# Performance work log

Hardware: AMD Instinct MI355X
Metric: run time of the kernel (lower is better)

## Reference

```python
import jax, jax.numpy as jnp
import numpy as np

B, N, DIM = 8, 8192, 512
H, DH = 8, 64
INNER = H * DH
EPS = 1e-5


def setup_inputs() -> dict:
    key = jax.random.key(0)
    ks = jax.random.split(key, 5)
    x = jax.random.normal(ks[0], (B, N, DIM), dtype=jnp.float32)
    w_qkv = jax.random.normal(ks[1], (DIM, 3 * INNER), dtype=jnp.float32) * (DIM ** -0.5)
    ln_w = jnp.ones((INNER,), dtype=jnp.float32)
    ln_b = jnp.zeros((INNER,), dtype=jnp.float32)
    w_out = jax.random.normal(ks[2], (INNER, DIM), dtype=jnp.float32) * (INNER ** -0.5)
    b_out = jnp.zeros((DIM,), dtype=jnp.float32)
    return {"x": x, "w_qkv": w_qkv, "ln_w": ln_w, "ln_b": ln_b,
            "w_out": w_out, "b_out": b_out}


def _layernorm(x, w, b):
    mu = jnp.mean(x, axis=-1, keepdims=True)
    var = jnp.mean(jnp.square(x - mu), axis=-1, keepdims=True)
    return (x - mu) * jax.lax.rsqrt(var + EPS) * w + b


def reference(x, w_qkv, ln_w, ln_b, w_out, b_out):
    b, n, _ = x.shape
    qkv = x @ w_qkv  # [b, n, 3*inner]
    q, k, v = jnp.split(qkv, 3, axis=-1)
    # b n (h d) -> b h n d
    def heads(t):
        return t.reshape(b, n, H, DH).transpose(0, 2, 1, 3)
    q, k, v = heads(q), heads(k), heads(v)
    q = jax.nn.relu(q)
    k = jax.nn.relu(k)
    kv = jnp.einsum('bhnm,bhnd->bhmd', k, v)   # [b, h, d, d]
    out = jnp.einsum('bhnm,bhmd->bhnd', q, kv)  # [b, h, n, d]
    out = out.transpose(0, 2, 1, 3).reshape(b, n, INNER)
    out = _layernorm(out, ln_w, ln_b)
    return out @ w_out + b_out
```

## Files before the change

kernel.cpp:

```cpp
#include <hip/hip_runtime.h>
#include <stdint.h>

#define B_ 8
#define N_ 8192
#define DIM_ 512
#define H_ 8
#define DH_ 64
#define ROWS (B_*N_)
#define TRIPLE (3*DIM_)
#define EPS_ 1e-5f

typedef __attribute__((ext_vector_type(8))) short short8;
typedef __attribute__((ext_vector_type(4))) float f32x4;
typedef __attribute__((ext_vector_type(4))) float fl4;
typedef __attribute__((ext_vector_type(4))) unsigned short us4;
typedef __attribute__((ext_vector_type(8))) unsigned short us8;

#define AS1 __attribute__((address_space(1)))
#define AS3 __attribute__((address_space(3)))

__device__ __forceinline__ void gld16(const void* g, void* l) {
    __builtin_amdgcn_global_load_lds((const AS1 void*)(uintptr_t)g,
                                     (AS3 void*)(unsigned)(uintptr_t)l, 16, 0, 0);
}

__device__ inline unsigned short f2bf(float f) {
    union { float f; unsigned int u; } x; x.f = f;
    unsigned int r = x.u + 0x7fffu + ((x.u >> 16) & 1u);
    return (unsigned short)(r >> 16);
}
__device__ inline float bf2f(unsigned short b) {
    union { unsigned int u; float f; } x; x.u = ((unsigned int)b) << 16;
    return x.f;
}

__device__ __forceinline__ int eoff(int row, int col) {
    return row * 64 + (col ^ ((((unsigned)row >> 2) & 3) << 4));
}

__global__ __launch_bounds__(256) void k_cvt(const float* __restrict__ x,
                                             unsigned short* __restrict__ xb) {
    size_t i = ((size_t)blockIdx.x * 256 + threadIdx.x) * 8;
    fl4 a = *(const fl4*)(x + i);
    fl4 b = *(const fl4*)(x + i + 4);
    us8 r;
    r[0] = f2bf(a[0]); r[1] = f2bf(a[1]); r[2] = f2bf(a[2]); r[3] = f2bf(a[3]);
    r[4] = f2bf(b[0]); r[5] = f2bf(b[1]); r[6] = f2bf(b[2]); r[7] = f2bf(b[3]);
    *(us8*)(xb + i) = r;
}

__global__ __launch_bounds__(256) void k_prep(const float* __restrict__ wq,
        const float* __restrict__ wo,
        unsigned short* __restrict__ wqT, unsigned short* __restrict__ woT) {
    __shared__ float T[32][33];
    int bid = blockIdx.x;
    const float* src; unsigned short* dst; int srcCols, dstCols, k0, n0;
    if (bid < 768) {
        int tn = bid % 48, tk = bid / 48;
        src = wq; dst = wqT; srcCols = 1536; dstCols = 512;
        k0 = tk * 32; n0 = tn * 32;
    } else {
        int b = bid - 768;
        int tn = b % 16, tk = b / 16;
        src = wo; dst = woT; srcCols = 512; dstCols = 512;
        k0 = tk * 32; n0 = tn * 32;
    }
    int t = threadIdx.x, r = t >> 3, c4 = (t & 7) * 4;
    fl4 v = *(const fl4*)(src + (size_t)(k0 + r) * srcCols + n0 + c4);
    T[c4 + 0][r] = v[0]; T[c4 + 1][r] = v[1];
    T[c4 + 2][r] = v[2]; T[c4 + 3][r] = v[3];
    __syncthreads();
    us4 o;
    o[0] = f2bf(T[r][c4 + 0]); o[1] = f2bf(T[r][c4 + 1]);
    o[2] = f2bf(T[r][c4 + 2]); o[3] = f2bf(T[r][c4 + 3]);
    *(us4*)(dst + (size_t)(n0 + r) * dstCols + k0 + c4) = o;
}

__global__ __launch_bounds__(512, 4) void k_qkv8(const unsigned short* __restrict__ xb,
        const unsigned short* __restrict__ wT,
        unsigned short* __restrict__ qkv)
{
    __shared__ __align__(1024) unsigned short LDSb[3][12288];

    const int tid  = threadIdx.x;
    const int lane = tid & 63;
    const int wid  = tid >> 6;
    const int wr   = wid >> 1;
    const int wc   = wid & 1;
    const int lr   = lane & 15;

    int id  = blockIdx.x;
    int nid = (id & 7) * 384 + (id >> 3);
    int n0  = (nid % 12) * 128;
    int m0  = (nid / 12) * 256;

    const unsigned short* pA[2];
    const unsigned short* pB1;
    unsigned ldstA[2], ldstB;
#pragma unroll
    for (int j = 0; j < 2; ++j) {
        int s    = tid + j * 512;
        int row  = ((s >> 6) << 4) + ((s >> 2) & 15);
        int colb = ((s & 3) << 4) ^ (((s >> 5) & 1) << 5);
        pA[j] = xb + (size_t)(m0 + row) * 512 + (colb >> 1);
        ldstA[j] = (unsigned)((j * 512 + wid * 64) * 8);
    }
    {
        int s    = tid;
        int row  = ((s >> 6) << 4) + ((s >> 2) & 15);
        int colb = ((s & 3) << 4) ^ (((s >> 5) & 1) << 5);
        pB1 = wT + (size_t)(n0 + row) * 512 + (colb >> 1);
        ldstB = (unsigned)(8192 + wid * 64 * 8);
    }
    const int kg = (lane >> 4) * 8;
    const int lo = lr * 32 + (kg ^ ((lr >> 3) << 4));

    auto STAGE = [&](int t, int slot) {
        gld16(pA[0] + t * 32, (void*)&LDSb[slot][ldstA[0]]);
        gld16(pA[1] + t * 32, (void*)&LDSb[slot][ldstA[1]]);
        gld16(pB1   + t * 32, (void*)&LDSb[slot][ldstB]);
    };

    f32x4 acc[4][4] = {};
    short8 af[4], bfr[4];

    STAGE(0, 0);
    STAGE(1, 1);

#define WAITV(n) asm volatile("s_waitcnt vmcnt(" #n ")" ::: "memory")
#pragma unroll
    for (int t = 0; t < 16; ++t) {
        if (t <= 14) WAITV(3);
        else         WAITV(0);
        __builtin_amdgcn_s_barrier();
        __builtin_amdgcn_sched_barrier(0);

        if (t + 2 < 16) STAGE(t + 2, (t + 2) % 3);

        const unsigned short* L = LDSb[t % 3];
#pragma unroll
        for (int m = 0; m < 4; ++m)
            af[m] = *(const short8*)&L[(wr * 4 + m) * 512 + lo];
#pragma unroll
        for (int n = 0; n < 4; ++n)
            bfr[n] = *(const short8*)&L[8192 + (wc * 4 + n) * 512 + lo];

        __builtin_amdgcn_s_setprio(1);
#pragma unroll
        for (int m = 0; m < 4; ++m)
#pragma unroll
            for (int n = 0; n < 4; ++n)
                acc[m][n] = __builtin_amdgcn_mfma_f32_16x16x32_bf16(af[m], bfr[n], acc[m][n], 0, 0, 0);
        __builtin_amdgcn_s_setprio(0);
    }
#undef WAITV

    __syncthreads();

    unsigned short* S = ((unsigned short*)LDSb) + wid * 4096;
    const bool relu_tile = (n0 < 1024);
#pragma unroll
    for (int m = 0; m < 4; ++m) {
        int rbase = m * 16 + ((lane >> 4) << 2);
#pragma unroll
        for (int n = 0; n < 4; ++n) {
            int col = n * 16 + lr;
#pragma unroll
            for (int r = 0; r < 4; ++r) {
                float v = acc[m][n][r];
                if (relu_tile && v < 0.0f) v = 0.0f;
                S[eoff(rbase + r, col)] = f2bf(v);
            }
        }
    }
    __syncthreads();
    {
        int rsub = lane >> 3, sub = lane & 7;
        size_t grow = (size_t)(m0 + wr * 64);
        int gcol = n0 + wc * 64 + sub * 8;
#pragma unroll
        for (int rd = 0; rd < 8; ++rd) {
            int row = rd * 8 + rsub;
            short8 vv = *(const short8*)&S[eoff(row, sub * 8)];
            *(short8*)(qkv + (grow + row) * TRIPLE + gcol) = vv;
        }
    }
}

__global__ __launch_bounds__(256) void k_qkv_f(const float* __restrict__ x,
        const unsigned short* __restrict__ wT,
        unsigned short* __restrict__ qkv)
{
    __shared__ unsigned short As[128][40];
    __shared__ unsigned short Bs[128][40];
    int t = threadIdx.x;
    int lane = t & 63, wave = t >> 6;
    int m0 = blockIdx.y * 128;
    int n0 = blockIdx.x * 128;
    int wm = (wave & 1) * 64, wn = (wave >> 1) * 64;
    int lr = lane & 15, kg = (lane >> 4) * 8;

    f32x4 acc[4][4] = {};
    for (int k0 = 0; k0 < DIM_; k0 += 32) {
#pragma unroll
        for (int i = 0; i < 4; ++i) {
            int c = t + 256 * i;
            int r = c >> 3, c4 = (c & 7) * 4;
            fl4 v = *(const fl4*)(x + (size_t)(m0 + r) * DIM_ + k0 + c4);
            unsigned short* dst = &As[r][c4];
            dst[0] = f2bf(v[0]); dst[1] = f2bf(v[1]); dst[2] = f2bf(v[2]); dst[3] = f2bf(v[3]);
        }
#pragma unroll
        for (int i = 0; i < 2; ++i) {
            int c = t + 256 * i;
            int r = c >> 2, c8 = (c & 3) * 8;
            *(int4*)&Bs[r][c8] = *(const int4*)(wT + (size_t)(n0 + r) * DIM_ + k0 + c8);
        }
        __syncthreads();
        short8 af[4], bfr[4];
#pragma unroll
        for (int i = 0; i < 4; ++i) af[i]  = *(short8*)&As[wm + i*16 + lr][kg];
#pragma unroll
        for (int j = 0; j < 4; ++j) bfr[j] = *(short8*)&Bs[wn + j*16 + lr][kg];
#pragma unroll
        for (int i = 0; i < 4; ++i)
#pragma unroll
            for (int j = 0; j < 4; ++j)
                acc[i][j] = __builtin_amdgcn_mfma_f32_16x16x32_bf16(af[i], bfr[j], acc[i][j], 0, 0, 0);
        __syncthreads();
    }
#pragma unroll
    for (int i = 0; i < 4; ++i) {
        int row = m0 + wm + i*16 + (lane >> 4) * 4;
#pragma unroll
        for (int j = 0; j < 4; ++j) {
            int col = n0 + wn + j*16 + (lane & 15);
            bool rl = (col < 1024);
#pragma unroll
            for (int r = 0; r < 4; ++r) {
                float v = acc[i][j][r];
                if (rl && v < 0.0f) v = 0.0f;
                qkv[(size_t)(row + r) * TRIPLE + col] = f2bf(v);
            }
        }
    }
}

__global__ __launch_bounds__(256) void k_kv(const unsigned short* __restrict__ qkv,
                                            float* __restrict__ kv)
{
    __shared__ unsigned short KT[64][136];
    __shared__ unsigned short VT[64][136];
    __shared__ float red[64 * 64];
    int t = threadIdx.x, lane = t & 63, wave = t >> 6;
    int bh = blockIdx.x;
    int b = bh >> 3, h = bh & 7;
    int chunk = blockIdx.y;
    size_t rowbase = (size_t)b * N_ + (size_t)chunk * 1024;
    int kcol = DIM_ + h * 64;
    int vcol = 2 * DIM_ + h * 64;
    int lr = lane & 15;

    f32x4 acc[4][4] = {};
    for (int tile = 0; tile < 8; ++tile) {
        size_t r0 = rowbase + tile * 128;
#pragma unroll
        for (int i = 0; i < 2; ++i) {
            int u = t + 256 * i;
            int rp = u >> 3;
            int c8 = (u & 7) * 8;
            size_t ra = r0 + 2 * rp, rb = ra + 1;
            us8 ka = *(const us8*)(qkv + ra * TRIPLE + kcol + c8);
            us8 kb = *(const us8*)(qkv + rb * TRIPLE + kcol + c8);
            us8 va = *(const us8*)(qkv + ra * TRIPLE + vcol + c8);
            us8 vb = *(const us8*)(qkv + rb * TRIPLE + vcol + c8);
#pragma unroll
            for (int j = 0; j < 8; ++j) {
                int d = c8 + j;
                *(unsigned int*)&KT[d][2 * rp] =
                    (unsigned int)ka[j] | ((unsigned int)kb[j] << 16);
                *(unsigned int*)&VT[d][2 * rp] =
                    (unsigned int)va[j] | ((unsigned int)vb[j] << 16);
            }
        }
        __syncthreads();
        int kg = wave * 32 + (lane >> 4) * 8;
        short8 af[4], bfr[4];
#pragma unroll
        for (int i = 0; i < 4; ++i) af[i]  = *(short8*)&KT[i*16 + lr][kg];
#pragma unroll
        for (int j = 0; j < 4; ++j) bfr[j] = *(short8*)&VT[j*16 + lr][kg];
#pragma unroll
        for (int i = 0; i < 4; ++i)
#pragma unroll
            for (int j = 0; j < 4; ++j)
                acc[i][j] = __builtin_amdgcn_mfma_f32_16x16x32_bf16(af[i], bfr[j], acc[i][j], 0, 0, 0);
        __syncthreads();
    }
    for (int w = 0; w < 4; ++w) {
        if (wave == w) {
#pragma unroll
            for (int i = 0; i < 4; ++i)
#pragma unroll
                for (int j = 0; j < 4; ++j)
#pragma unroll
                    for (int r = 0; r < 4; ++r) {
                        int m = i*16 + (lane >> 4) * 4 + r;
                        int d = j*16 + (lane & 15);
                        if (w == 0) red[m * 64 + d] = acc[i][j][r];
                        else        red[m * 64 + d] += acc[i][j][r];
                    }
        }
        __syncthreads();
    }
    float* kvout = kv + (size_t)bh * 4096;
#pragma unroll
    for (int i = 0; i < 16; ++i) {
        int idx = t + 256 * i;
        atomicAdd(&kvout[idx], red[idx]);
    }
}

__global__ __launch_bounds__(256) void k_kvt(const float* __restrict__ kv,
                                             unsigned short* __restrict__ kvtb) {
    __shared__ float T[64][65];
    int bh = blockIdx.x, t = threadIdx.x;
    const float* src = kv + (size_t)bh * 4096;
    unsigned short* dst = kvtb + (size_t)bh * 4096;
#pragma unroll
    for (int i = 0; i < 16; ++i) {
        int idx = t + 256 * i;
        T[idx & 63][idx >> 6] = src[idx];
    }
    __syncthreads();
#pragma unroll
    for (int i = 0; i < 16; ++i) {
        int idx = t + 256 * i;
        dst[idx] = f2bf(T[idx >> 6][idx & 63]);
    }
}

__global__ __launch_bounds__(256) void k_attn(unsigned short* __restrict__ qkv,
                                              const unsigned short* __restrict__ kvtb,
                                              const float* __restrict__ lnw,
                                              const float* __restrict__ lnb)
{
    __shared__ unsigned short Qh[128][72];
    __shared__ unsigned short kvT[64][72];
    __shared__ __align__(64) unsigned short Sout[128 * 64];
    __shared__ float muS[128], rsS[128];
    int t = threadIdx.x, lane = t & 63, wave = t >> 6;
    size_t r0 = (size_t)blockIdx.x * 128;
    int b = (int)(r0 / N_);
    int lr = lane & 15;

    float lw8[8], lb8[8];
#pragma unroll
    for (int j = 0; j < 8; ++j) { lw8[j] = lnw[lane * 8 + j]; lb8[j] = lnb[lane * 8 + j]; }

    float s8[8] = {}, ss8[8] = {};

    for (int h = 0; h < H_; ++h) {
#pragma unroll
        for (int i = 0; i < 4; ++i) {
            int c = t + 256 * i;
            int r = c >> 3, f8 = (c & 7) * 8;
            *(us8*)&Qh[r][f8] = *(const us8*)(qkv + (r0 + r) * TRIPLE + h * 64 + f8);
        }
        const unsigned short* kvh = kvtb + (size_t)(b * 8 + h) * 4096;
#pragma unroll
        for (int i = 0; i < 2; ++i) {
            int c = t + 256 * i;
            int d = c >> 3, m8 = (c & 7) * 8;
            *(us8*)&kvT[d][m8] = *(const us8*)(kvh + d * 64 + m8);
        }
        __syncthreads();
        f32x4 acc[2][4] = {};
#pragma unroll
        for (int ks = 0; ks < 2; ++ks) {
            int kg = ks * 32 + (lane >> 4) * 8;
            short8 af[2], bfr[4];
#pragma unroll
            for (int i = 0; i < 2; ++i) af[i]  = *(short8*)&Qh[wave*32 + i*16 + lr][kg];
#pragma unroll
            for (int j = 0; j < 4; ++j) bfr[j] = *(short8*)&kvT[j*16 + lr][kg];
#pragma unroll
            for (int i = 0; i < 2; ++i)
#pragma unroll
                for (int j = 0; j < 4; ++j)
                    acc[i][j] = __builtin_amdgcn_mfma_f32_16x16x32_bf16(af[i], bfr[j], acc[i][j], 0, 0, 0);
        }
#pragma unroll
        for (int i = 0; i < 2; ++i)
#pragma unroll
            for (int j = 0; j < 4; ++j) {
                int rbase = wave*32 + i*16 + (lane >> 4) * 4;
                int col = j*16 + lr;
#pragma unroll
                for (int r = 0; r < 4; ++r) {
                    float v = acc[i][j][r];
                    s8[i*4+r]  += v;
                    ss8[i*4+r] += v * v;
                    Sout[eoff(rbase + r, col)] = f2bf(v);
                }
            }
        __syncthreads();
        {
            int sub = t & 7, rsub = t >> 3;
#pragma unroll
            for (int rd = 0; rd < 4; ++rd) {
                int row = rd * 32 + rsub;
                short8 vv = *(const short8*)&Sout[eoff(row, sub * 8)];
                *(short8*)(qkv + (r0 + row) * TRIPLE + h * 64 + sub * 8) = vv;
            }
        }
        __syncthreads();
    }

#pragma unroll
    for (int q = 0; q < 8; ++q) {
        float s = s8[q], ss = ss8[q];
        s += __shfl_xor(s, 1);  ss += __shfl_xor(ss, 1);
        s += __shfl_xor(s, 2);  ss += __shfl_xor(ss, 2);
        s += __shfl_xor(s, 4);  ss += __shfl_xor(ss, 4);
        s += __shfl_xor(s, 8);  ss += __shfl_xor(ss, 8);
        s8[q] = s; ss8[q] = ss;
    }
    if (lr == 0) {
#pragma unroll
        for (int q = 0; q < 8; ++q) {
            int row = wave*32 + (q >> 2)*16 + (lane >> 4)*4 + (q & 3);
            float m = s8[q] * (1.0f / 512.0f);
            muS[row] = m;
            rsS[row] = rsqrtf(ss8[q] * (1.0f / 512.0f) - m * m + EPS_);
        }
    }
    __syncthreads();

#pragma unroll
    for (int i = 0; i < 32; ++i) {
        int row = wave + 4 * i;
        unsigned short* p = qkv + (r0 + row) * TRIPLE + lane * 8;
        us8 v = *(const us8*)p;
        float mm = muS[row], rr = rsS[row];
        us8 o;
#pragma unroll
        for (int j = 0; j < 8; ++j)
            o[j] = f2bf((bf2f(v[j]) - mm) * rr * lw8[j] + lb8[j]);
        *(us8*)p = o;
    }
}

__global__ __launch_bounds__(256) void k_out(const unsigned short* __restrict__ qkv,
        const unsigned short* __restrict__ woutT,
        const float* __restrict__ bout, float* __restrict__ out)
{
    __shared__ unsigned short As[128][40];
    __shared__ unsigned short Bs[128][40];
    int t = threadIdx.x, lane = t & 63, wave = t >> 6;
    int id  = blockIdx.y * 4 + blockIdx.x;
    int nid = (id & 7) * 256 + (id >> 3);
    int m0  = (nid >> 2) * 128;
    int n0  = (nid & 3) * 128;
    int wm = (wave & 1) * 64, wn = (wave >> 1) * 64;
    int lr = lane & 15, kg = (lane >> 4) * 8;

    f32x4 acc[4][4] = {};
    for (int k0 = 0; k0 < 512; k0 += 32) {
#pragma unroll
        for (int i = 0; i < 2; ++i) {
            int c = t + 256 * i;
            int r = c >> 2, c8 = (c & 3) * 8;
            *(int4*)&As[r][c8] = *(const int4*)(qkv + (size_t)(m0 + r) * TRIPLE + k0 + c8);
        }
#pragma unroll
        for (int i = 0; i < 2; ++i) {
            int c = t + 256 * i;
            int r = c >> 2, c8 = (c & 3) * 8;
            *(int4*)&Bs[r][c8] = *(const int4*)(woutT + (size_t)(n0 + r) * DIM_ + k0 + c8);
        }
        __syncthreads();
        short8 af[4], bfr[4];
#pragma unroll
        for (int i = 0; i < 4; ++i) af[i]  = *(short8*)&As[wm + i*16 + lr][kg];
#pragma unroll
        for (int j = 0; j < 4; ++j) bfr[j] = *(short8*)&Bs[wn + j*16 + lr][kg];
#pragma unroll
        for (int i = 0; i < 4; ++i)
#pragma unroll
            for (int j = 0; j < 4; ++j)
                acc[i][j] = __builtin_amdgcn_mfma_f32_16x16x32_bf16(af[i], bfr[j], acc[i][j], 0, 0, 0);
        __syncthreads();
    }
#pragma unroll
    for (int i = 0; i < 4; ++i) {
        int row = m0 + wm + i*16 + (lane >> 4) * 4;
#pragma unroll
        for (int j = 0; j < 4; ++j) {
            int col = n0 + wn + j*16 + (lane & 15);
            float bo = bout[col];
#pragma unroll
            for (int r = 0; r < 4; ++r)
                out[(size_t)(row + r) * DIM_ + col] = acc[i][j][r] + bo;
        }
    }
}

extern "C" void kernel_launch(void* const* d_in, const int* in_sizes, int n_in,
                              void* d_out, int out_size, void* d_ws, size_t ws_size,
                              hipStream_t stream) {
    (void)in_sizes; (void)n_in; (void)out_size;
    const float* x     = (const float*)d_in[0];
    const float* w_qkv = (const float*)d_in[1];
    const float* ln_w  = (const float*)d_in[2];
    const float* ln_b  = (const float*)d_in[3];
    const float* w_out = (const float*)d_in[4];
    const float* b_out = (const float*)d_in[5];
    float* out = (float*)d_out;

    char* ws = (char*)d_ws;
    const size_t QKV_BYTES = (size_t)ROWS * TRIPLE * sizeof(unsigned short);
    const size_t KV_BYTES  = (size_t)64 * 64 * 64 * sizeof(float);
    const size_t WQT_BYTES = (size_t)TRIPLE * DIM_ * sizeof(unsigned short);
    const size_t WOT_BYTES = (size_t)DIM_ * DIM_ * sizeof(unsigned short);
    const size_t KVT_BYTES = (size_t)64 * 64 * 64 * sizeof(unsigned short);
    const size_t XB_BYTES  = (size_t)ROWS * DIM_ * sizeof(unsigned short);
    unsigned short* qkv   = (unsigned short*)ws;
    float*          kvbuf = (float*)(ws + QKV_BYTES);
    unsigned short* wqkvT = (unsigned short*)(ws + QKV_BYTES + KV_BYTES);
    unsigned short* woutT = (unsigned short*)(ws + QKV_BYTES + KV_BYTES + WQT_BYTES);
    unsigned short* kvtb  = (unsigned short*)(ws + QKV_BYTES + KV_BYTES + WQT_BYTES + WOT_BYTES);
    unsigned short* xb    = (unsigned short*)(ws + QKV_BYTES + KV_BYTES + WQT_BYTES + WOT_BYTES + KVT_BYTES);
    const size_t NEED = QKV_BYTES + KV_BYTES + WQT_BYTES + WOT_BYTES + KVT_BYTES + XB_BYTES;

    hipMemsetAsync(kvbuf, 0, KV_BYTES, stream);
    k_prep<<<1024, 256, 0, stream>>>(w_qkv, w_out, wqkvT, woutT);
    if (ws_size >= NEED) {
        k_cvt<<<16384, 256, 0, stream>>>(x, xb);
        k_qkv8<<<dim3(3072), 512, 0, stream>>>(xb, wqkvT, qkv);
    } else {
        k_qkv_f<<<dim3(12, 512), 256, 0, stream>>>(x, wqkvT, qkv);
    }
    k_kv<<<dim3(64, 8), 256, 0, stream>>>(qkv, kvbuf);
    k_kvt<<<64, 256, 0, stream>>>(kvbuf, kvtb);
    k_attn<<<512, 256, 0, stream>>>(qkv, kvtb, ln_w, ln_b);
    k_out<<<dim3(4, 512), 256, 0, stream>>>(qkv, woutT, b_out, out);
}
```

Baseline: 525.8 us.

## Fuse attention output, layernorm and output projection into one kernel

Merges k_attn and k_out into a single kernel. Each 128-row block keeps its full 128x512 attention output in a swizzled LDS buffer, applies layernorm in place, then runs the output GEMM against w_out read straight from global memory. This removes the write and re-read of the normalized activations through qkv and one kernel launch. In exchange it uses 128KB+ of LDS per block, so occupancy drops to about one block per CU. Q, kv and w_out fragments are now loaded from global memory directly rather than staged through shared memory.

```diff
diff --git a/kernel.cpp b/kernel.cpp
--- a/kernel.cpp
+++ b/kernel.cpp
@@ -36,6 +36,10 @@
 
 __device__ __forceinline__ int eoff(int row, int col) {
     return row * 64 + (col ^ ((((unsigned)row >> 2) & 3) << 4));
+}
+
+__device__ __forceinline__ int aoff(int row, int col) {
+    return row * 512 + ((((col >> 3) ^ (row & 7)) << 3) | (col & 7));
 }
 
 __global__ __launch_bounds__(256) void k_cvt(const float* __restrict__ x,
@@ -340,50 +344,38 @@
     }
 }
 
-__global__ __launch_bounds__(256) void k_attn(unsigned short* __restrict__ qkv,
-                                              const unsigned short* __restrict__ kvtb,
-                                              const float* __restrict__ lnw,
-                                              const float* __restrict__ lnb)
+__global__ __launch_bounds__(256) void k_ao(
+        const unsigned short* __restrict__ qkv,
+        const unsigned short* __restrict__ kvtb,
+        const float* __restrict__ lnw, const float* __restrict__ lnb,
+        const unsigned short* __restrict__ woutT,
+        const float* __restrict__ bout, float* __restrict__ out)
 {
-    __shared__ unsigned short Qh[128][72];
-    __shared__ unsigned short kvT[64][72];
-    __shared__ __align__(64) unsigned short Sout[128 * 64];
-    __shared__ float muS[128], rsS[128];
+    __shared__ unsigned short attnS[128 * 512];
+    __shared__ float lwS[512], lbS[512], muS[128], rsS[128];
     int t = threadIdx.x, lane = t & 63, wave = t >> 6;
+    int lr = lane & 15;
     size_t r0 = (size_t)blockIdx.x * 128;
     int b = (int)(r0 / N_);
-    int lr = lane & 15;
-
-    float lw8[8], lb8[8];
-#pragma unroll
-    for (int j = 0; j < 8; ++j) { lw8[j] = lnw[lane * 8 + j]; lb8[j] = lnb[lane * 8 + j]; }
+
+    for (int i = t; i < 512; i += 256) { lwS[i] = lnw[i]; lbS[i] = lnb[i]; }
 
     float s8[8] = {}, ss8[8] = {};
 
+#pragma unroll
     for (int h = 0; h < H_; ++h) {
-#pragma unroll
-        for (int i = 0; i < 4; ++i) {
-            int c = t + 256 * i;
-            int r = c >> 3, f8 = (c & 7) * 8;
-            *(us8*)&Qh[r][f8] = *(const us8*)(qkv + (r0 + r) * TRIPLE + h * 64 + f8);
-        }
         const unsigned short* kvh = kvtb + (size_t)(b * 8 + h) * 4096;
-#pragma unroll
-        for (int i = 0; i < 2; ++i) {
-            int c = t + 256 * i;
-            int d = c >> 3, m8 = (c & 7) * 8;
-            *(us8*)&kvT[d][m8] = *(const us8*)(kvh + d * 64 + m8);
-        }
-        __syncthreads();
         f32x4 acc[2][4] = {};
 #pragma unroll
         for (int ks = 0; ks < 2; ++ks) {
             int kg = ks * 32 + (lane >> 4) * 8;
             short8 af[2], bfr[4];
 #pragma unroll
-            for (int i = 0; i < 2; ++i) af[i]  = *(short8*)&Qh[wave*32 + i*16 + lr][kg];
-#pragma unroll
-            for (int j = 0; j < 4; ++j) bfr[j] = *(short8*)&kvT[j*16 + lr][kg];
+            for (int i = 0; i < 2; ++i)
+                af[i] = *(const short8*)(qkv + (r0 + wave * 32 + i * 16 + lr) * TRIPLE + h * 64 + kg);
+#pragma unroll
+            for (int j = 0; j < 4; ++j)
+                bfr[j] = *(const short8*)(kvh + (j * 16 + lr) * 64 + kg);
 #pragma unroll
             for (int i = 0; i < 2; ++i)
 #pragma unroll
@@ -394,27 +386,16 @@
         for (int i = 0; i < 2; ++i)
 #pragma unroll
             for (int j = 0; j < 4; ++j) {
-                int rbase = wave*32 + i*16 + (lane >> 4) * 4;
-                int col = j*16 + lr;
+                int rbase = wave * 32 + i * 16 + (lane >> 4) * 4;
+                int col = h * 64 + j * 16 + lr;
 #pragma unroll
                 for (int r = 0; r < 4; ++r) {
                     float v = acc[i][j][r];
-                    s8[i*4+r]  += v;
-                    ss8[i*4+r] += v * v;
-                    Sout[eoff(rbase + r, col)] = f2bf(v);
+                    s8[i * 4 + r] += v;
+                    ss8[i * 4 + r] += v * v;
+                    attnS[aoff(rbase + r, col)] = f2bf(v);
                 }
             }
-        __syncthreads();
-        {
-            int sub = t & 7, rsub = t >> 3;
-#pragma unroll
-            for (int rd = 0; rd < 4; ++rd) {
-                int row = rd * 32 + rsub;
-                short8 vv = *(const short8*)&Sout[eoff(row, sub * 8)];
-                *(short8*)(qkv + (r0 + row) * TRIPLE + h * 64 + sub * 8) = vv;
-            }
-        }
-        __syncthreads();
     }
 
 #pragma unroll
@@ -429,7 +410,7 @@
     if (lr == 0) {
 #pragma unroll
         for (int q = 0; q < 8; ++q) {
-            int row = wave*32 + (q >> 2)*16 + (lane >> 4)*4 + (q & 3);
+            int row = wave * 32 + (q >> 2) * 16 + (lane >> 4) * 4 + (q & 3);
             float m = s8[q] * (1.0f / 512.0f);
             muS[row] = m;
             rsS[row] = rsqrtf(ss8[q] * (1.0f / 512.0f) - m * m + EPS_);
@@ -437,71 +418,55 @@
     }
     __syncthreads();
 
-#pragma unroll
-    for (int i = 0; i < 32; ++i) {
-        int row = wave + 4 * i;
-        unsigned short* p = qkv + (r0 + row) * TRIPLE + lane * 8;
-        us8 v = *(const us8*)p;
+    {
+        int row = t >> 1, ch = (t & 1) * 32;
         float mm = muS[row], rr = rsS[row];
-        us8 o;
-#pragma unroll
-        for (int j = 0; j < 8; ++j)
-            o[j] = f2bf((bf2f(v[j]) - mm) * rr * lw8[j] + lb8[j]);
-        *(us8*)p = o;
-    }
-}
-
-__global__ __launch_bounds__(256) void k_out(const unsigned short* __restrict__ qkv,
-        const unsigned short* __restrict__ woutT,
-        const float* __restrict__ bout, float* __restrict__ out)
-{
-    __shared__ unsigned short As[128][40];
-    __shared__ unsigned short Bs[128][40];
-    int t = threadIdx.x, lane = t & 63, wave = t >> 6;
-    int id  = blockIdx.y * 4 + blockIdx.x;
-    int nid = (id & 7) * 256 + (id >> 3);
-    int m0  = (nid >> 2) * 128;
-    int n0  = (nid & 3) * 128;
-    int wm = (wave & 1) * 64, wn = (wave >> 1) * 64;
-    int lr = lane & 15, kg = (lane >> 4) * 8;
-
-    f32x4 acc[4][4] = {};
-    for (int k0 = 0; k0 < 512; k0 += 32) {
-#pragma unroll
-        for (int i = 0; i < 2; ++i) {
-            int c = t + 256 * i;
-            int r = c >> 2, c8 = (c & 3) * 8;
-            *(int4*)&As[r][c8] = *(const int4*)(qkv + (size_t)(m0 + r) * TRIPLE + k0 + c8);
-        }
-#pragma unroll
-        for (int i = 0; i < 2; ++i) {
-            int c = t + 256 * i;
-            int r = c >> 2, c8 = (c & 3) * 8;
-            *(int4*)&Bs[r][c8] = *(const int4*)(woutT + (size_t)(n0 + r) * DIM_ + k0 + c8);
-        }
-        __syncthreads();
-        short8 af[4], bfr[4];
-#pragma unroll
-        for (int i = 0; i < 4; ++i) af[i]  = *(short8*)&As[wm + i*16 + lr][kg];
-#pragma unroll
-        for (int j = 0; j < 4; ++j) bfr[j] = *(short8*)&Bs[wn + j*16 + lr][kg];
-#pragma unroll
-        for (int i = 0; i < 4; ++i)
+        unsigned short* base = attnS + row * 512;
+#pragma unroll
+        for (int g = 0; g < 32; ++g) {
+            int colg = ch + g;
+            us8* p = (us8*)(base + ((colg ^ (row & 7)) << 3));
+            us8 v = *p, o;
+#pragma unroll
+            for (int j = 0; j < 8; ++j)
+                o[j] = f2bf((bf2f(v[j]) - mm) * rr * lwS[colg * 8 + j] + lbS[colg * 8 + j]);
+            *p = o;
+        }
+    }
+    __syncthreads();
+
+#pragma unroll
+    for (int nc = 0; nc < 2; ++nc) {
+        int ncol = wave * 128 + nc * 64;
+        f32x4 acc[8][4] = {};
+        for (int k0 = 0; k0 < 512; k0 += 32) {
+            int gk = (k0 >> 3) + (lane >> 4);
+            short8 af[8], bfr[4];
+#pragma unroll
+            for (int m = 0; m < 8; ++m) {
+                int row = m * 16 + lr;
+                af[m] = *(const short8*)&attnS[row * 512 + ((gk ^ (row & 7)) << 3)];
+            }
 #pragma unroll
             for (int j = 0; j < 4; ++j)
-                acc[i][j] = __builtin_amdgcn_mfma_f32_16x16x32_bf16(af[i], bfr[j], acc[i][j], 0, 0, 0);
-        __syncthreads();
-    }
-#pragma unroll
-    for (int i = 0; i < 4; ++i) {
-        int row = m0 + wm + i*16 + (lane >> 4) * 4;
-#pragma unroll
-        for (int j = 0; j < 4; ++j) {
-            int col = n0 + wn + j*16 + (lane & 15);
-            float bo = bout[col];
-#pragma unroll
-            for (int r = 0; r < 4; ++r)
-                out[(size_t)(row + r) * DIM_ + col] = acc[i][j][r] + bo;
+                bfr[j] = *(const short8*)(woutT + (size_t)(ncol + j * 16 + lr) * 512 + k0 + (lane >> 4) * 8);
+#pragma unroll
+            for (int m = 0; m < 8; ++m)
+#pragma unroll
+                for (int j = 0; j < 4; ++j)
+                    acc[m][j] = __builtin_amdgcn_mfma_f32_16x16x32_bf16(af[m], bfr[j], acc[m][j], 0, 0, 0);
+        }
+#pragma unroll
+        for (int m = 0; m < 8; ++m) {
+            size_t row = r0 + m * 16 + ((lane >> 4) << 2);
+#pragma unroll
+            for (int j = 0; j < 4; ++j) {
+                int col = ncol + j * 16 + (lane & 15);
+                float bo = bout[col];
+#pragma unroll
+                for (int r = 0; r < 4; ++r)
+                    out[(row + r) * DIM_ + col] = acc[m][j][r] + bo;
+            }
         }
     }
 }
@@ -543,6 +508,5 @@
     }
     k_kv<<<dim3(64, 8), 256, 0, stream>>>(qkv, kvbuf);
     k_kvt<<<64, 256, 0, stream>>>(kvbuf, kvtb);
-    k_attn<<<512, 256, 0, stream>>>(qkv, kvtb, ln_w, ln_b);
-    k_out<<<dim3(4, 512), 256, 0, stream>>>(qkv, woutT, b_out, out);
-}
+    k_ao<<<512, 256, 0, stream>>>(qkv, kvtb, ln_w, ln_b, woutT, b_out, out);
+}
```

Result: faster. 493.9 us (-6.1%).
